# Optimization experiments

Measured on AMD Instinct MI355X. Metric: run time of the kernel, lower is better.

Reference implementation:

```python
import math
import jax, jax.numpy as jnp
import numpy as np

D_MODEL = 1024
N_HEADS = 16
D_K = D_MODEL // N_HEADS


def _alibi_slopes(n_heads):
    # Faithful to the torch _get_slopes: slopes[i] = 2**(-8 + i), subsampled if
    # n_heads is not a power of two.
    power = 2 ** math.ceil(math.log2(n_heads))
    slopes = np.array([2.0 ** (-8 + i) for i in range(power)], dtype=np.float32)
    if n_heads != power:
        ratio = power // n_heads
        slopes = slopes[np.arange(0, power, ratio)][:n_heads]
    return jnp.asarray(slopes)


def setup_inputs() -> dict:
    key = jax.random.key(0)
    ks = jax.random.split(key, 11)
    B, S, D = 2, 2048, D_MODEL
    w = 0.02  # weight init scale
    return {
        "query": jax.random.normal(ks[0], (B, S, D), jnp.float32),
        "key": jax.random.normal(ks[1], (B, S, D), jnp.float32),
        "value": jax.random.normal(ks[2], (B, S, D), jnp.float32),
        "Wq": jax.random.normal(ks[3], (D, D), jnp.float32) * w,
        "bq": jax.random.normal(ks[4], (D,), jnp.float32) * w,
        "Wk": jax.random.normal(ks[5], (D, D), jnp.float32) * w,
        "bk": jax.random.normal(ks[6], (D,), jnp.float32) * w,
        "Wv": jax.random.normal(ks[7], (D, D), jnp.float32) * w,
        "bv": jax.random.normal(ks[8], (D,), jnp.float32) * w,
        "Wo": jax.random.normal(ks[9], (D, D), jnp.float32) * w,
        "bo": jax.random.normal(ks[10], (D,), jnp.float32) * w,
    }


def reference(query, key, value, Wq, bq, Wk, bk, Wv, bv, Wo, bo):
    B, Sq, D = query.shape
    Sk = key.shape[1]
    H, dk = N_HEADS, D_K

    # projections (torch Linear: x @ W.T + b)
    q = (query @ Wq.T + bq).reshape(B, Sq, H, dk).transpose(0, 2, 1, 3)  # [B,H,Sq,dk]
    k = (key @ Wk.T + bk).reshape(B, Sk, H, dk).transpose(0, 2, 1, 3)    # [B,H,Sk,dk]
    v = (value @ Wv.T + bv).reshape(B, Sk, H, dk).transpose(0, 2, 1, 3)  # [B,H,Sk,dk]

    scores = jnp.einsum("bhqd,bhkd->bhqk", q, k) / jnp.sqrt(jnp.float32(dk))

    # ALiBi bias: slopes[h] * (i - j), non-causal path (is_causal=False)
    dist = (jnp.arange(Sq)[:, None] - jnp.arange(Sk)[None, :]).astype(scores.dtype)
    slopes = _alibi_slopes(H)
    scores = scores + slopes[None, :, None, None] * dist[None, None, :, :]

    attn = jax.nn.softmax(scores, axis=-1)
    out = jnp.einsum("bhqk,bhkd->bhqd", attn, v)          # [B,H,Sq,dk]
    out = out.transpose(0, 2, 1, 3).reshape(B, Sq, D)     # [B,Sq,D]
    return out @ Wo.T + bo
```

## Files before the change

kernel.cpp:

```cpp
#include <hip/hip_runtime.h>

typedef __bf16 bf16_t;
typedef bf16_t bf16x8 __attribute__((ext_vector_type(8)));
typedef float f32x4 __attribute__((ext_vector_type(4)));
typedef float f32x16 __attribute__((ext_vector_type(16)));
typedef unsigned short u16x4 __attribute__((ext_vector_type(4)));
typedef unsigned int u32x4v __attribute__((ext_vector_type(4)));
typedef unsigned int u32;

#define DEV static __device__ __forceinline__


DEV unsigned short f2bf(float f) {
  unsigned int u = __builtin_bit_cast(unsigned int, f);
  u = (u + 0x7fffu + ((u >> 16) & 1u)) >> 16;
  return (unsigned short)u;
}

DEV float fexp2(float x) {
  float r;
  asm("v_exp_f32 %0, %1" : "=v"(r) : "v"(x));
  return r;
}

DEV u32 cvtpk(float lo, float hi_) {
  u32 r;
  asm("v_cvt_pk_bf16_f32 %0, %1, %2" : "=v"(r) : "v"(lo), "v"(hi_));
  return r;
}

DEV void plswap(u32& a, u32& b) {
  asm("v_permlane32_swap_b32 %0, %1" : "+v"(a), "+v"(b));
}

DEV void async_ld16(const unsigned short* gsrc, unsigned short* lbase, int lane) {
#if __has_builtin(__builtin_amdgcn_global_load_lds)
  __builtin_amdgcn_global_load_lds(
      (const __attribute__((address_space(1))) unsigned int*)(const void*)gsrc,
      (__attribute__((address_space(3))) unsigned int*)(void*)lbase, 16, 0, 0);
#else
  *reinterpret_cast<u32x4v*>(reinterpret_cast<char*>(lbase) + lane * 16) =
      *reinterpret_cast<const u32x4v*>(gsrc);
#endif
}


DEV void cvt_body(const float* __restrict__ src, unsigned short* __restrict__ dst, int i) {
  const float4* s = reinterpret_cast<const float4*>(src) + (size_t)i * 2;
  float4 a = s[0], c = s[1];
  u16x4 lo = {f2bf(a.x), f2bf(a.y), f2bf(a.z), f2bf(a.w)};
  u16x4 hi = {f2bf(c.x), f2bf(c.y), f2bf(c.z), f2bf(c.w)};
  u16x4* d = reinterpret_cast<u16x4*>(dst) + (size_t)i * 2;
  d[0] = lo;
  d[1] = hi;
}

__global__ __launch_bounds__(256) void cvt_all(
    const float* __restrict__ q, const float* __restrict__ k, const float* __restrict__ v,
    const float* __restrict__ Wq, const float* __restrict__ Wk, const float* __restrict__ Wv,
    const float* __restrict__ Wo, unsigned short* dq, unsigned short* dk, unsigned short* dv,
    unsigned short* dWq, unsigned short* dWk, unsigned short* dWv, unsigned short* dWo,
    unsigned* __restrict__ nb2z) {
  const int bid = blockIdx.x;
  if (nb2z != nullptr && bid == 0 && threadIdx.x < 64) nb2z[threadIdx.x] = 0u;
  const float* src;
  unsigned short* dst;
  int i;
  if (bid < 6144) {
    const int z = bid >> 11;
    src = z == 0 ? q : z == 1 ? k : v;
    dst = z == 0 ? dq : z == 1 ? dk : dv;
    i = (bid & 2047) * 256 + threadIdx.x;
  } else {
    const int z = (bid - 6144) >> 9;
    src = z == 0 ? Wq : z == 1 ? Wk : z == 2 ? Wv : Wo;
    dst = z == 0 ? dWq : z == 1 ? dWk : z == 2 ? dWv : dWo;
    i = ((bid - 6144) & 511) * 256 + threadIdx.x;
  }
  cvt_body(src, dst, i);
}


DEV void mfma_step(const unsigned short* lA, const unsigned short* lB, int lane, int wm, int wn,
                   f32x4 acc[4][4]) {
#pragma unroll
  for (int kk = 0; kk < 2; ++kk) {
    bf16x8 af[4], bfr[4];
#pragma unroll
    for (int f = 0; f < 4; ++f) {
      const int rowA = wm * 64 + f * 16 + (lane & 15);
      const int cA = (kk * 4 + (lane >> 4)) ^ (rowA & 7);
      af[f] = *reinterpret_cast<const bf16x8*>(lA + rowA * 64 + cA * 8);
      const int rowB = wn * 64 + f * 16 + (lane & 15);
      const int cB = (kk * 4 + (lane >> 4)) ^ (rowB & 7);
      bfr[f] = *reinterpret_cast<const bf16x8*>(lB + rowB * 64 + cB * 8);
    }
#pragma unroll
    for (int i = 0; i < 4; ++i)
#pragma unroll
      for (int j = 0; j < 4; ++j)
        acc[i][j] = __builtin_amdgcn_mfma_f32_16x16x32_bf16(af[i], bfr[j], acc[i][j], 0, 0, 0);
  }
}

DEV void gemm_core(const unsigned short* __restrict__ X, const unsigned short* __restrict__ W,
                   unsigned short* lA0, unsigned short* lA1, unsigned short* lB0,
                   unsigned short* lB1, int bm0, int bn0, int lane, int wv, int wm, int wn,
                   f32x4 acc[4][4]) {
  const unsigned short* pa[4];
  const unsigned short* pb[4];
#pragma unroll
  for (int r = 0; r < 4; ++r) {
    const int row = (r * 4 + wv) * 8 + (lane >> 3);
    const int chunk = (lane & 7) ^ (row & 7);
    pa[r] = X + (size_t)(bm0 + row) * 1024 + chunk * 8;
    pb[r] = W + (size_t)(bn0 + row) * 1024 + chunk * 8;
  }
#pragma unroll
  for (int r = 0; r < 4; ++r) {
    async_ld16(pa[r], lA0 + (r * 4 + wv) * 512, lane);
    async_ld16(pb[r], lB0 + (r * 4 + wv) * 512, lane);
  }
  __syncthreads();
#pragma unroll
  for (int kt = 0; kt < 16; ++kt) {
    const unsigned short* lA = (kt & 1) ? lA1 : lA0;
    const unsigned short* lB = (kt & 1) ? lB1 : lB0;
    unsigned short* nA = (kt & 1) ? lA0 : lA1;
    unsigned short* nB = (kt & 1) ? lB0 : lB1;
    if (kt < 15) {
#pragma unroll
      for (int r = 0; r < 4; ++r) {
        async_ld16(pa[r] + (kt + 1) * 64, nA + (r * 4 + wv) * 512, lane);
        async_ld16(pb[r] + (kt + 1) * 64, nB + (r * 4 + wv) * 512, lane);
      }
    }
    mfma_step(lA, lB, lane, wm, wn, acc);
    __syncthreads();
  }
}


__global__ __launch_bounds__(256) void gemm_qkv_kernel(
    const unsigned short* __restrict__ Xq, const unsigned short* __restrict__ Xk,
    const unsigned short* __restrict__ Xv, const unsigned short* __restrict__ Wq,
    const unsigned short* __restrict__ Wk, const unsigned short* __restrict__ Wv,
    const float* __restrict__ bq, const float* __restrict__ bk, const float* __restrict__ bv,
    unsigned short* __restrict__ Qp, unsigned short* __restrict__ Kp,
    unsigned short* __restrict__ Vp, unsigned* __restrict__ nb2) {
  __shared__ unsigned short lA[2][8192];
  __shared__ unsigned short lB[2][8192];
  const unsigned short* X;
  const unsigned short* W;
  const float* bias;
  unsigned short* dst;
  if (blockIdx.z == 0) { X = Xq; W = Wq; bias = bq; dst = Qp; }
  else if (blockIdx.z == 1) { X = Xk; W = Wk; bias = bk; dst = Kp; }
  else { X = Xv; W = Wv; bias = bv; dst = Vp; }
  const bool zV = (blockIdx.z == 2);
  const bool zK = (blockIdx.z == 1) && (nb2 != nullptr);
  const int lane = threadIdx.x & 63, wv = threadIdx.x >> 6;
  const int wm = wv >> 1, wn = wv & 1;
  const int bm0 = blockIdx.x * 128, bn0 = blockIdx.y * 128;
  f32x4 acc[4][4] = {};
  gemm_core(X, W, lA[0], lA[1], lB[0], lB[1], bm0, bn0, lane, wv, wm, wn, acc);
  float rowmax = 0.0f;
#pragma unroll
  for (int i = 0; i < 4; ++i) {
    const int mbase = bm0 + wm * 64 + i * 16 + ((lane >> 4) << 2);
#pragma unroll
    for (int r = 0; r < 4; ++r) {
      const int m = mbase + r;
      const int b = m >> 11, s = m & 2047;
      float ssp = 0.0f;
#pragma unroll
      for (int j = 0; j < 4; ++j) {
        const int n = bn0 + wn * 64 + j * 16 + (lane & 15);
        const float val = acc[i][j][r] + bias[n];
        const unsigned short v16 = f2bf(val);
        const int h = n >> 6, d = n & 63;
        if (zV)
          dst[((size_t)(b * 16 + h) * 64 + d) * 2048 + s] = v16;
        else
          dst[((size_t)(b * 16 + h) * 2048 + s) * 64 + d] = v16;
        ssp = __builtin_fmaf(val, val, ssp);
      }
      if (zK) {
        ssp += __shfl_xor(ssp, 1);
        ssp += __shfl_xor(ssp, 2);
        ssp += __shfl_xor(ssp, 4);
        ssp += __shfl_xor(ssp, 8);
        rowmax = fmaxf(rowmax, ssp);
      }
    }
  }
  if (zK) {
    rowmax = fmaxf(rowmax, __shfl_xor(rowmax, 16));
    rowmax = fmaxf(rowmax, __shfl_xor(rowmax, 32));
    if (lane == 0) {
      const int bh = (bm0 >> 11) * 16 + blockIdx.y * 2 + wn;
      atomicMax(nb2 + bh, __float_as_uint(rowmax));
    }
  }
}


__global__ __launch_bounds__(256) void gemm_out_kernel(const unsigned short* __restrict__ X,
                                                       const unsigned short* __restrict__ W,
                                                       const float* __restrict__ bias,
                                                       float* __restrict__ out) {
  __shared__ unsigned short lA[2][8192];
  __shared__ unsigned short lB[2][8192];
  const int lane = threadIdx.x & 63, wv = threadIdx.x >> 6;
  const int wm = wv >> 1, wn = wv & 1;
  const int bm0 = blockIdx.x * 128, bn0 = blockIdx.y * 128;
  f32x4 acc[4][4] = {};
  gemm_core(X, W, lA[0], lA[1], lB[0], lB[1], bm0, bn0, lane, wv, wm, wn, acc);
#pragma unroll
  for (int i = 0; i < 4; ++i) {
    const int mbase = bm0 + wm * 64 + i * 16 + ((lane >> 4) << 2);
#pragma unroll
    for (int j = 0; j < 4; ++j) {
      const int n = bn0 + wn * 64 + j * 16 + (lane & 15);
      const float bia = bias[n];
#pragma unroll
      for (int r = 0; r < 4; ++r) out[(size_t)(mbase + r) * 1024 + n] = acc[i][j][r] + bia;
    }
  }
}


__global__ __launch_bounds__(256) void knorm_kernel(const unsigned short* __restrict__ Kp,
                                                    unsigned* __restrict__ nb2) {
  const int bh = blockIdx.y;
  const int s = blockIdx.x * 256 + threadIdx.x;
  const u32x4v* row = reinterpret_cast<const u32x4v*>(Kp + ((size_t)bh * 2048 + s) * 64);
  float ss = 0.0f;
#pragma unroll
  for (int c = 0; c < 8; ++c) {
    u32x4v u = row[c];
#pragma unroll
    for (int e = 0; e < 4; ++e) {
      const float lo = __builtin_bit_cast(float, u[e] << 16);
      const float hi = __builtin_bit_cast(float, u[e] & 0xFFFF0000u);
      ss = __builtin_fmaf(lo, lo, ss);
      ss = __builtin_fmaf(hi, hi, ss);
    }
  }
#pragma unroll
  for (int off = 1; off <= 32; off <<= 1) ss = fmaxf(ss, __shfl_xor(ss, off));
  if ((threadIdx.x & 63) == 0) atomicMax(nb2 + bh, __float_as_uint(ss));
}


DEV void stage_tile64(const unsigned short* __restrict__ Gbase, size_t stride, int colbase,
                      unsigned short* lbuf, int lane, int wv) {
#pragma unroll
  for (int i = 0; i < 4; ++i) {
    const int r = i * 16 + wv * 8 + (lane >> 3);
    const int chunk = (lane & 7) ^ (r & 7);
    async_ld16(Gbase + (size_t)r * stride + colbase + chunk * 8, lbuf + (i * 16 + wv * 8) * 64,
               lane);
  }
}

__global__ __launch_bounds__(128) void attn_split_kernel(
    const unsigned short* __restrict__ Qp, const unsigned short* __restrict__ Kp,
    const unsigned short* __restrict__ VTp, const unsigned* __restrict__ nb2,
    float* __restrict__ ML, float* __restrict__ Opart, int Ct, int nsplit) {
  __shared__ unsigned short Kb[2][64 * 64];
  __shared__ unsigned short Vb[2][64 * 64];
  __shared__ float sred[4];
  const int lane = threadIdx.x & 63, wv = threadIdx.x >> 6;
  const int lq = lane & 31, hi = lane >> 5;
  const int qt = blockIdx.x, sp = blockIdx.y, bh = blockIdx.z;
  const int h = bh & 15;
  const int idx = bh * 32 + qt;
  const float L2E = 1.4426950408889634f;
  const float slope2 = ldexpf(L2E, h - 8);
  const float SC2 = 0.125f * L2E;
  const int t0 = sp * Ct;
  float* mlb = ML + ((size_t)idx * nsplit + sp) * 128;
  const size_t headoff = (size_t)bh * 2048 * 64;
  const unsigned short* Qh = Qp + headoff;
  const unsigned short* Kh = Kp + headoff;
  const unsigned short* VTh = VTp + headoff;
  const int q_glob = qt * 64 + wv * 32 + lq;

  float cb0[16], cb1[16];
#pragma unroll
  for (int r = 0; r < 16; ++r) {
    cb0[r] = -slope2 * (float)(4 * hi + (r & 3) + 8 * (r >> 2));
    cb1[r] = cb0[r] - slope2 * 32.0f;
  }

  bf16x8 qf[4];
#pragma unroll
  for (int tt = 0; tt < 4; ++tt)
    qf[tt] = *reinterpret_cast<const bf16x8*>(Qh + (size_t)q_glob * 64 + tt * 16 + hi * 8);

  stage_tile64(Kh + (size_t)(t0 * 64) * 64, 64, 0, Kb[0], lane, wv);
  stage_tile64(VTh, 2048, t0 * 64, Vb[0], lane, wv);

  float qq = 0.0f;
#pragma unroll
  for (int tt = 0; tt < 4; ++tt)
#pragma unroll
    for (int e = 0; e < 8; ++e) {
      const float x = (float)qf[tt][e];
      qq = __builtin_fmaf(x, x, qq);
    }
  qq += __shfl_xor(qq, 32);
#pragma unroll
  for (int off = 1; off <= 16; off <<= 1) qq = fmaxf(qq, __shfl_xor(qq, off));
  {
    f32x16 s0 = {}, s1 = {};
#pragma unroll
    for (int tt = 0; tt < 4; ++tt) {
      bf16x8 k0 = *reinterpret_cast<const bf16x8*>(Kh + (size_t)lq * 64 + tt * 16 + hi * 8);
      s0 = __builtin_amdgcn_mfma_f32_32x32x16_bf16(k0, qf[tt], s0, 0, 0, 0);
      bf16x8 k1 =
          *reinterpret_cast<const bf16x8*>(Kh + (size_t)(32 + lq) * 64 + tt * 16 + hi * 8);
      s1 = __builtin_amdgcn_mfma_f32_32x32x16_bf16(k1, qf[tt], s1, 0, 0, 0);
    }
    float zmax = -3.0e38f;
#pragma unroll
    for (int r = 0; r < 16; ++r) {
      const float x0 = __builtin_fmaf(s0[r], SC2, cb0[r]);
      const float x1 = __builtin_fmaf(s1[r], SC2, cb1[r]);
      zmax = fmaxf(zmax, fmaxf(x0, x1));
    }
    zmax = fmaxf(zmax, __shfl_xor(zmax, 32));
    float zmin = zmax;
#pragma unroll
    for (int off = 1; off <= 16; off <<= 1) zmin = fminf(zmin, __shfl_xor(zmin, off));
    if (lane == 0) {
      sred[wv] = zmin;
      sred[2 + wv] = qq;
    }
  }
  __syncthreads();
  const float m_floor = fminf(sred[0], sred[1]);
  const float qn = sqrtf(fmaxf(sred[2], sred[3]));
  const float blt = qn * sqrtf(__uint_as_float(nb2[bh])) * SC2;
  const float tf = (blt - m_floor + 34.0f) / (slope2 * 64.0f);
  const int T_act = min(32, (int)tf + 1);
  const int nt = min(Ct, T_act - t0);
  if (nt <= 0) {
    mlb[threadIdx.x] = threadIdx.x < 64 ? -3.0e38f : 0.0f;
    return;
  }
  float* ob = Opart + ((size_t)idx * nsplit + sp) * 4096;

  f32x16 acc0 = {}, acc1 = {};
  float m_run = m_floor, l_run = 0.0f;

  for (int ti = 0; ti < nt; ++ti) {
    const int kv0 = (t0 + ti) * 64;
    const float s2k = slope2 * (float)kv0;
    const unsigned short* Kc = Kb[ti & 1];
    const unsigned short* Vc = Vb[ti & 1];
    if (ti + 1 < nt) {
      stage_tile64(Kh + (size_t)(kv0 + 64) * 64, 64, 0, Kb[(ti + 1) & 1], lane, wv);
      stage_tile64(VTh, 2048, kv0 + 64, Vb[(ti + 1) & 1], lane, wv);
    }
    f32x16 s0 = {}, s1 = {};
    __builtin_amdgcn_s_setprio(1);
#pragma unroll
    for (int tt = 0; tt < 4; ++tt) {
      {
        const int row = lq;
        const int ch = (tt * 2 + hi) ^ (row & 7);
        bf16x8 kf = *reinterpret_cast<const bf16x8*>(Kc + row * 64 + ch * 8);
        s0 = __builtin_amdgcn_mfma_f32_32x32x16_bf16(kf, qf[tt], s0, 0, 0, 0);
      }
      {
        const int row = 32 + lq;
        const int ch = (tt * 2 + hi) ^ (row & 7);
        bf16x8 kf = *reinterpret_cast<const bf16x8*>(Kc + row * 64 + ch * 8);
        s1 = __builtin_amdgcn_mfma_f32_32x32x16_bf16(kf, qf[tt], s1, 0, 0, 0);
      }
    }
    __builtin_amdgcn_s_setprio(0);
    float zmax = -3.0e38f;
#pragma unroll
    for (int r = 0; r < 16; ++r) {
      s0[r] = __builtin_fmaf(s0[r], SC2, cb0[r]);
      s1[r] = __builtin_fmaf(s1[r], SC2, cb1[r]);
      zmax = fmaxf(zmax, fmaxf(s0[r], s1[r]));
    }
    zmax = fmaxf(zmax, __shfl_xor(zmax, 32));
    const float tmax_true = zmax - s2k;
    if (__any(tmax_true > m_run + 8.0f)) {
      const float m_new = fmaxf(m_run, tmax_true);
      const float alpha = fexp2(m_run - m_new);
      m_run = m_new;
      l_run *= alpha;
      acc0 *= alpha;
      acc1 *= alpha;
    }
    const float mm = m_run + s2k;
    float ps0 = 0.0f, ps1 = 0.0f;
#pragma unroll
    for (int r = 0; r < 16; ++r) {
      const float p0 = fexp2(s0[r] - mm);
      const float p1 = fexp2(s1[r] - mm);
      s0[r] = p0;
      s1[r] = p1;
      ps0 += p0;
      ps1 += p1;
    }
    float psum = ps0 + ps1;
    psum += __shfl_xor(psum, 32);
    l_run += psum;
    bf16x8 pf[4];
#pragma unroll
    for (int half = 0; half < 2; ++half) {
      u32 w0 = cvtpk(s0[half * 8 + 0], s0[half * 8 + 1]);
      u32 w2 = cvtpk(s0[half * 8 + 4], s0[half * 8 + 5]);
      plswap(w0, w2);
      u32 w1 = cvtpk(s0[half * 8 + 2], s0[half * 8 + 3]);
      u32 w3 = cvtpk(s0[half * 8 + 6], s0[half * 8 + 7]);
      plswap(w1, w3);
      u32x4v ww = {w0, w1, w2, w3};
      pf[half] = __builtin_bit_cast(bf16x8, ww);
    }
#pragma unroll
    for (int half = 0; half < 2; ++half) {
      u32 w0 = cvtpk(s1[half * 8 + 0], s1[half * 8 + 1]);
      u32 w2 = cvtpk(s1[half * 8 + 4], s1[half * 8 + 5]);
      plswap(w0, w2);
      u32 w1 = cvtpk(s1[half * 8 + 2], s1[half * 8 + 3]);
      u32 w3 = cvtpk(s1[half * 8 + 6], s1[half * 8 + 7]);
      plswap(w1, w3);
      u32x4v ww = {w0, w1, w2, w3};
      pf[2 + half] = __builtin_bit_cast(bf16x8, ww);
    }
    __builtin_amdgcn_s_setprio(1);
#pragma unroll
    for (int tt = 0; tt < 4; ++tt) {
      {
        const int row = lq;
        const int ch = (tt * 2 + hi) ^ (row & 7);
        bf16x8 vf = *reinterpret_cast<const bf16x8*>(Vc + row * 64 + ch * 8);
        acc0 = __builtin_amdgcn_mfma_f32_32x32x16_bf16(vf, pf[tt], acc0, 0, 0, 0);
      }
      {
        const int row = 32 + lq;
        const int ch = (tt * 2 + hi) ^ (row & 7);
        bf16x8 vf = *reinterpret_cast<const bf16x8*>(Vc + row * 64 + ch * 8);
        acc1 = __builtin_amdgcn_mfma_f32_32x32x16_bf16(vf, pf[tt], acc1, 0, 0, 0);
      }
    }
    __builtin_amdgcn_s_setprio(0);
    __syncthreads();
  }
  const int qloc = wv * 32 + lq;
  if (hi == 0) {
    mlb[qloc] = m_run;
    mlb[64 + qloc] = l_run;
  }
#pragma unroll
  for (int g = 0; g < 4; ++g) {
    f32x4 w0, w1;
#pragma unroll
    for (int e = 0; e < 4; ++e) {
      w0[e] = acc0[g * 4 + e];
      w1[e] = acc1[g * 4 + e];
    }
    *reinterpret_cast<f32x4*>(ob + qloc * 64 + g * 8 + 4 * hi) = w0;
    *reinterpret_cast<f32x4*>(ob + qloc * 64 + 32 + g * 8 + 4 * hi) = w1;
  }
}


__global__ __launch_bounds__(256) void attn_combine(const float* __restrict__ ML,
                                                    const float* __restrict__ Opart,
                                                    unsigned short* __restrict__ Ob, int nsplit) {
  const int idx = blockIdx.x;
  const int bh = idx >> 5, qt = idx & 31;
  const int h = bh & 15, b = bh >> 4;
  const int q = threadIdx.x >> 2, d0 = (threadIdx.x & 3) * 16;
  const float* mlb = ML + (size_t)idx * nsplit * 128;
  const float* ob = Opart + (size_t)idx * nsplit * 4096;
  float m_g = -3.0e38f;
  for (int s = 0; s < nsplit; ++s) m_g = fmaxf(m_g, mlb[s * 128 + q]);
  float l = 0.0f;
  f32x4 acc[4] = {};
  for (int s = 0; s < nsplit; ++s) {
    const float ms = mlb[s * 128 + q], ls = mlb[s * 128 + 64 + q];
    const float w = fexp2(ms - m_g);
    const float wl = w * ls;
    if (wl > 0.0f) {
      l += wl;
      const f32x4* src = reinterpret_cast<const f32x4*>(ob + (size_t)s * 4096 + q * 64 + d0);
#pragma unroll
      for (int j = 0; j < 4; ++j) {
        f32x4 v = src[j];
#pragma unroll
        for (int e = 0; e < 4; ++e) acc[j][e] = __builtin_fmaf(w, v[e], acc[j][e]);
      }
    }
  }
  const float invl = 1.0f / l;
  unsigned short* orow = Ob + ((size_t)(b * 2048 + qt * 64 + q)) * 1024 + h * 64 + d0;
#pragma unroll
  for (int j = 0; j < 4; ++j) {
    u16x4 pk;
#pragma unroll
    for (int e = 0; e < 4; ++e) pk[e] = f2bf(acc[j][e] * invl);
    *reinterpret_cast<u16x4*>(orow + j * 4) = pk;
  }
}


extern "C" void kernel_launch(void* const* d_in, const int* in_sizes, int n_in, void* d_out,
                              int out_size, void* d_ws, size_t ws_size, hipStream_t stream) {
  const float* q = (const float*)d_in[0];
  const float* k = (const float*)d_in[1];
  const float* v = (const float*)d_in[2];
  const float* Wq = (const float*)d_in[3];
  const float* bq = (const float*)d_in[4];
  const float* Wk = (const float*)d_in[5];
  const float* bk = (const float*)d_in[6];
  const float* Wv = (const float*)d_in[7];
  const float* bv = (const float*)d_in[8];
  const float* Wo = (const float*)d_in[9];
  const float* bo = (const float*)d_in[10];

  char* ws = (char*)d_ws;
  const size_t MB = 1024 * 1024;
  unsigned short* qb = (unsigned short*)(ws + 0 * MB);
  unsigned short* kb = (unsigned short*)(ws + 8 * MB);
  unsigned short* vb = (unsigned short*)(ws + 16 * MB);
  unsigned short* Wqb = (unsigned short*)(ws + 24 * MB);
  unsigned short* Wkb = (unsigned short*)(ws + 26 * MB);
  unsigned short* Wvb = (unsigned short*)(ws + 28 * MB);
  unsigned short* Wob = (unsigned short*)(ws + 30 * MB);
  unsigned short* Qp = (unsigned short*)(ws + 32 * MB);
  unsigned short* Kp = (unsigned short*)(ws + 40 * MB);
  unsigned short* VTp = (unsigned short*)(ws + 48 * MB);
  unsigned short* Obf = (unsigned short*)(ws + 0 * MB);

  int nsplit;
  float *ML, *Opart;
  unsigned* nb2;
  bool fold_knorm;
  if (ws_size >= (size_t)121 * MB) nsplit = 4;
  else if (ws_size >= (size_t)89 * MB) nsplit = 2;
  else nsplit = 1;
  if (ws_size >= (size_t)73 * MB) {
    fold_knorm = true;
    nb2 = (unsigned*)(ws + 56 * MB);
    ML = (float*)(ws + 26 * MB + 65536);
    Opart = (float*)(ws + 56 * MB + 4096);
  } else {
    fold_knorm = false;
    nsplit = 1;
    nb2 = (unsigned*)(ws + 26 * MB);
    ML = (float*)(ws + 26 * MB + 65536);
    Opart = (float*)(ws + 8 * MB);
  }
  const int Ct = 32 / nsplit;

  cvt_all<<<8192, 256, 0, stream>>>(q, k, v, Wq, Wk, Wv, Wo, qb, kb, vb, Wqb, Wkb, Wvb, Wob,
                                    fold_knorm ? nb2 : nullptr);
  gemm_qkv_kernel<<<dim3(32, 8, 3), 256, 0, stream>>>(qb, kb, vb, Wqb, Wkb, Wvb, bq, bk, bv, Qp,
                                                      Kp, VTp, fold_knorm ? nb2 : nullptr);
  if (!fold_knorm) {
    hipMemsetAsync(nb2, 0, 64 * sizeof(unsigned), stream);
    knorm_kernel<<<dim3(8, 32), 256, 0, stream>>>(Kp, nb2);
  }
  attn_split_kernel<<<dim3(32, nsplit, 32), 128, 0, stream>>>(Qp, Kp, VTp, nb2, ML, Opart, Ct,
                                                              nsplit);
  attn_combine<<<1024, 256, 0, stream>>>(ML, Opart, Obf, nsplit);
  gemm_out_kernel<<<dim3(32, 8), 256, 0, stream>>>(Obf, Wob, bo, (float*)d_out);
}
```

Measured before the change: 124.4 us.

## Enlarge QKV projection GEMM tiles to 256x256 with 512-thread blocks

The QKV projection GEMM moves from 128x128 tiles with 4 waves to 256x256 tiles with 8 waves, each wave computing a 128x64 sub-tile. This halves global loads per output element and raises arithmetic intensity per LDS stage. In exchange, LDS use doubles to 128KB per block and the grid shrinks to 192 blocks, fewer than the CU count, so occupancy and load balance may suffer. The output GEMM keeps the old 128-tile path, its loop no longer fully unrolled.

New measurement: 135.9 us. 9.3% more time.

```diff
diff --git a/kernel.cpp b/kernel.cpp
--- a/kernel.cpp
+++ b/kernel.cpp
@@ -81,75 +81,74 @@
 }
 
 
-DEV void mfma_step(const unsigned short* lA, const unsigned short* lB, int lane, int wm, int wn,
-                   f32x4 acc[4][4]) {
+DEV void stage_tile256(const unsigned short* __restrict__ G, int row0, int k0,
+                       unsigned short* lbuf, int lane, int w) {
+#pragma unroll
+  for (int r = 0; r < 4; ++r) {
+    const int row = r * 64 + w * 8 + (lane >> 3);
+    const int chunk = (lane & 7) ^ (row & 7);
+    async_ld16(G + (size_t)(row0 + row) * 1024 + k0 + chunk * 8, lbuf + (r * 64 + w * 8) * 64,
+               lane);
+  }
+}
+
+DEV void mfma_step256(const unsigned short* lA, const unsigned short* lB, int lane, int wm,
+                      int wn, f32x4 acc[8][4]) {
 #pragma unroll
   for (int kk = 0; kk < 2; ++kk) {
-    bf16x8 af[4], bfr[4];
-#pragma unroll
-    for (int f = 0; f < 4; ++f) {
-      const int rowA = wm * 64 + f * 16 + (lane & 15);
+    bf16x8 af[8], bfr[4];
+#pragma unroll
+    for (int f = 0; f < 8; ++f) {
+      const int rowA = wm * 128 + f * 16 + (lane & 15);
       const int cA = (kk * 4 + (lane >> 4)) ^ (rowA & 7);
       af[f] = *reinterpret_cast<const bf16x8*>(lA + rowA * 64 + cA * 8);
-      const int rowB = wn * 64 + f * 16 + (lane & 15);
+    }
+#pragma unroll
+    for (int j = 0; j < 4; ++j) {
+      const int rowB = wn * 64 + j * 16 + (lane & 15);
       const int cB = (kk * 4 + (lane >> 4)) ^ (rowB & 7);
-      bfr[f] = *reinterpret_cast<const bf16x8*>(lB + rowB * 64 + cB * 8);
-    }
-#pragma unroll
-    for (int i = 0; i < 4; ++i)
+      bfr[j] = *reinterpret_cast<const bf16x8*>(lB + rowB * 64 + cB * 8);
+    }
+#pragma unroll
+    for (int i = 0; i < 8; ++i)
 #pragma unroll
       for (int j = 0; j < 4; ++j)
         acc[i][j] = __builtin_amdgcn_mfma_f32_16x16x32_bf16(af[i], bfr[j], acc[i][j], 0, 0, 0);
   }
 }
 
-DEV void gemm_core(const unsigned short* __restrict__ X, const unsigned short* __restrict__ W,
-                   unsigned short* lA0, unsigned short* lA1, unsigned short* lB0,
-                   unsigned short* lB1, int bm0, int bn0, int lane, int wv, int wm, int wn,
-                   f32x4 acc[4][4]) {
-  const unsigned short* pa[4];
-  const unsigned short* pb[4];
-#pragma unroll
-  for (int r = 0; r < 4; ++r) {
-    const int row = (r * 4 + wv) * 8 + (lane >> 3);
-    const int chunk = (lane & 7) ^ (row & 7);
-    pa[r] = X + (size_t)(bm0 + row) * 1024 + chunk * 8;
-    pb[r] = W + (size_t)(bn0 + row) * 1024 + chunk * 8;
-  }
-#pragma unroll
-  for (int r = 0; r < 4; ++r) {
-    async_ld16(pa[r], lA0 + (r * 4 + wv) * 512, lane);
-    async_ld16(pb[r], lB0 + (r * 4 + wv) * 512, lane);
-  }
+DEV void gemm_core256(const unsigned short* __restrict__ X, const unsigned short* __restrict__ W,
+                      unsigned short* lA0, unsigned short* lA1, unsigned short* lB0,
+                      unsigned short* lB1, int bm0, int bn0, int lane, int w, int wm, int wn,
+                      f32x4 acc[8][4]) {
+  stage_tile256(X, bm0, 0, lA0, lane, w);
+  stage_tile256(W, bn0, 0, lB0, lane, w);
   __syncthreads();
-#pragma unroll
+#pragma unroll 2
   for (int kt = 0; kt < 16; ++kt) {
     const unsigned short* lA = (kt & 1) ? lA1 : lA0;
     const unsigned short* lB = (kt & 1) ? lB1 : lB0;
     unsigned short* nA = (kt & 1) ? lA0 : lA1;
     unsigned short* nB = (kt & 1) ? lB0 : lB1;
     if (kt < 15) {
-#pragma unroll
-      for (int r = 0; r < 4; ++r) {
-        async_ld16(pa[r] + (kt + 1) * 64, nA + (r * 4 + wv) * 512, lane);
-        async_ld16(pb[r] + (kt + 1) * 64, nB + (r * 4 + wv) * 512, lane);
-      }
-    }
-    mfma_step(lA, lB, lane, wm, wn, acc);
+      stage_tile256(X, bm0, (kt + 1) * 64, nA, lane, w);
+      stage_tile256(W, bn0, (kt + 1) * 64, nB, lane, w);
+    }
+    mfma_step256(lA, lB, lane, wm, wn, acc);
     __syncthreads();
   }
 }
 
 
-__global__ __launch_bounds__(256) void gemm_qkv_kernel(
+__global__ __launch_bounds__(512, 2) void gemm_qkv_kernel(
     const unsigned short* __restrict__ Xq, const unsigned short* __restrict__ Xk,
     const unsigned short* __restrict__ Xv, const unsigned short* __restrict__ Wq,
     const unsigned short* __restrict__ Wk, const unsigned short* __restrict__ Wv,
     const float* __restrict__ bq, const float* __restrict__ bk, const float* __restrict__ bv,
     unsigned short* __restrict__ Qp, unsigned short* __restrict__ Kp,
     unsigned short* __restrict__ Vp, unsigned* __restrict__ nb2) {
-  __shared__ unsigned short lA[2][8192];
-  __shared__ unsigned short lB[2][8192];
+  __shared__ unsigned short lA[2][16384];
+  __shared__ unsigned short lB[2][16384];
   const unsigned short* X;
   const unsigned short* W;
   const float* bias;
@@ -159,15 +158,15 @@
   else { X = Xv; W = Wv; bias = bv; dst = Vp; }
   const bool zV = (blockIdx.z == 2);
   const bool zK = (blockIdx.z == 1) && (nb2 != nullptr);
-  const int lane = threadIdx.x & 63, wv = threadIdx.x >> 6;
-  const int wm = wv >> 1, wn = wv & 1;
-  const int bm0 = blockIdx.x * 128, bn0 = blockIdx.y * 128;
-  f32x4 acc[4][4] = {};
-  gemm_core(X, W, lA[0], lA[1], lB[0], lB[1], bm0, bn0, lane, wv, wm, wn, acc);
+  const int lane = threadIdx.x & 63, w = threadIdx.x >> 6;
+  const int wm = w >> 2, wn = w & 3;
+  const int bm0 = blockIdx.x * 256, bn0 = blockIdx.y * 256;
+  f32x4 acc[8][4] = {};
+  gemm_core256(X, W, lA[0], lA[1], lB[0], lB[1], bm0, bn0, lane, w, wm, wn, acc);
   float rowmax = 0.0f;
 #pragma unroll
-  for (int i = 0; i < 4; ++i) {
-    const int mbase = bm0 + wm * 64 + i * 16 + ((lane >> 4) << 2);
+  for (int i = 0; i < 8; ++i) {
+    const int mbase = bm0 + wm * 128 + i * 16 + ((lane >> 4) << 2);
 #pragma unroll
     for (int r = 0; r < 4; ++r) {
       const int m = mbase + r;
@@ -198,9 +197,64 @@
     rowmax = fmaxf(rowmax, __shfl_xor(rowmax, 16));
     rowmax = fmaxf(rowmax, __shfl_xor(rowmax, 32));
     if (lane == 0) {
-      const int bh = (bm0 >> 11) * 16 + blockIdx.y * 2 + wn;
+      const int bh = (bm0 >> 11) * 16 + blockIdx.y * 4 + wn;
       atomicMax(nb2 + bh, __float_as_uint(rowmax));
     }
+  }
+}
+
+
+DEV void stage_b128(const unsigned short* __restrict__ G, int row0, int k0,
+                    unsigned short* lbuf, int lane, int wv) {
+#pragma unroll
+  for (int r = 0; r < 4; ++r) {
+    const int rowB = (r * 4 + wv) * 8 + (lane >> 3);
+    const int chunk = (lane & 7) ^ (rowB & 7);
+    async_ld16(G + (size_t)(row0 + rowB) * 1024 + k0 + chunk * 8, lbuf + (r * 4 + wv) * 512,
+               lane);
+  }
+}
+
+DEV void mfma_step(const unsigned short* lA, const unsigned short* lB, int lane, int wm, int wn,
+                   f32x4 acc[4][4]) {
+#pragma unroll
+  for (int kk = 0; kk < 2; ++kk) {
+    bf16x8 af[4], bfr[4];
+#pragma unroll
+    for (int f = 0; f < 4; ++f) {
+      const int rowA = wm * 64 + f * 16 + (lane & 15);
+      const int cA = (kk * 4 + (lane >> 4)) ^ (rowA & 7);
+      af[f] = *reinterpret_cast<const bf16x8*>(lA + rowA * 64 + cA * 8);
+      const int rowB = wn * 64 + f * 16 + (lane & 15);
+      const int cB = (kk * 4 + (lane >> 4)) ^ (rowB & 7);
+      bfr[f] = *reinterpret_cast<const bf16x8*>(lB + rowB * 64 + cB * 8);
+    }
+#pragma unroll
+    for (int i = 0; i < 4; ++i)
+#pragma unroll
+      for (int j = 0; j < 4; ++j)
+        acc[i][j] = __builtin_amdgcn_mfma_f32_16x16x32_bf16(af[i], bfr[j], acc[i][j], 0, 0, 0);
+  }
+}
+
+DEV void gemm_core(const unsigned short* __restrict__ X, const unsigned short* __restrict__ W,
+                   unsigned short* lA0, unsigned short* lA1, unsigned short* lB0,
+                   unsigned short* lB1, int bm0, int bn0, int lane, int wv, int wm, int wn,
+                   f32x4 acc[4][4]) {
+  stage_b128(X, bm0, 0, lA0, lane, wv);
+  stage_b128(W, bn0, 0, lB0, lane, wv);
+  __syncthreads();
+  for (int kt = 0; kt < 16; ++kt) {
+    const unsigned short* lA = (kt & 1) ? lA1 : lA0;
+    const unsigned short* lB = (kt & 1) ? lB1 : lB0;
+    unsigned short* nA = (kt & 1) ? lA0 : lA1;
+    unsigned short* nB = (kt & 1) ? lB0 : lB1;
+    if (kt < 15) {
+      stage_b128(X, bm0, (kt + 1) * 64, nA, lane, wv);
+      stage_b128(W, bn0, (kt + 1) * 64, nB, lane, wv);
+    }
+    mfma_step(lA, lB, lane, wm, wn, acc);
+    __syncthreads();
   }
 }
 
@@ -565,7 +619,7 @@
 
   cvt_all<<<8192, 256, 0, stream>>>(q, k, v, Wq, Wk, Wv, Wo, qb, kb, vb, Wqb, Wkb, Wvb, Wob,
                                     fold_knorm ? nb2 : nullptr);
-  gemm_qkv_kernel<<<dim3(32, 8, 3), 256, 0, stream>>>(qb, kb, vb, Wqb, Wkb, Wvb, bq, bk, bv, Qp,
+  gemm_qkv_kernel<<<dim3(16, 4, 3), 512, 0, stream>>>(qb, kb, vb, Wqb, Wkb, Wvb, bq, bk, bv, Qp,
                                                       Kp, VTp, fold_knorm ? nb2 : nullptr);
   if (!fold_knorm) {
     hipMemsetAsync(nb2, 0, 64 * sizeof(unsigned), stream);
```

## Rewrite QKV projection GEMM as 256x256 tile, 8-wave ping-pong pipeline

Applied to the files above, without the earlier changes.

The QKV projection GEMM moves from 128x128 tiles with 4 waves and a double buffer to 256x256 tiles with 8 waves. Half-tiles are staged through a four-slot LDS ring, and loads are interleaved with MFMA groups between barriers. Explicit vmcnt waits, s_setprio around the MFMA bursts and sched_barrier fences keep memory traffic overlapped with compute. The larger tile gives more reuse per LDS load, but the grid shrinks to 192 blocks at one block per CU, which may leave some of the 256 CUs idle. It also uses more LDS and registers.

After: 145.2 us. 1.17x slower.

```diff
diff --git a/kernel.cpp b/kernel.cpp
--- a/kernel.cpp
+++ b/kernel.cpp
@@ -81,75 +81,56 @@
 }
 
 
-DEV void mfma_step(const unsigned short* lA, const unsigned short* lB, int lane, int wm, int wn,
-                   f32x4 acc[4][4]) {
-#pragma unroll
-  for (int kk = 0; kk < 2; ++kk) {
-    bf16x8 af[4], bfr[4];
-#pragma unroll
-    for (int f = 0; f < 4; ++f) {
-      const int rowA = wm * 64 + f * 16 + (lane & 15);
-      const int cA = (kk * 4 + (lane >> 4)) ^ (rowA & 7);
-      af[f] = *reinterpret_cast<const bf16x8*>(lA + rowA * 64 + cA * 8);
-      const int rowB = wn * 64 + f * 16 + (lane & 15);
-      const int cB = (kk * 4 + (lane >> 4)) ^ (rowB & 7);
-      bfr[f] = *reinterpret_cast<const bf16x8*>(lB + rowB * 64 + cB * 8);
-    }
-#pragma unroll
-    for (int i = 0; i < 4; ++i)
-#pragma unroll
-      for (int j = 0; j < 4; ++j)
-        acc[i][j] = __builtin_amdgcn_mfma_f32_16x16x32_bf16(af[i], bfr[j], acc[i][j], 0, 0, 0);
-  }
-}
-
-DEV void gemm_core(const unsigned short* __restrict__ X, const unsigned short* __restrict__ W,
-                   unsigned short* lA0, unsigned short* lA1, unsigned short* lB0,
-                   unsigned short* lB1, int bm0, int bn0, int lane, int wv, int wm, int wn,
-                   f32x4 acc[4][4]) {
-  const unsigned short* pa[4];
-  const unsigned short* pb[4];
-#pragma unroll
-  for (int r = 0; r < 4; ++r) {
-    const int row = (r * 4 + wv) * 8 + (lane >> 3);
+DEV void stage_half(const unsigned short* __restrict__ G, int grow0, int k0,
+                    unsigned short* hbuf, int tid) {
+  const int lane = tid & 63, w = tid >> 6;
+#pragma unroll
+  for (int l = 0; l < 2; ++l) {
+    const int row = l * 64 + w * 8 + (lane >> 3);
     const int chunk = (lane & 7) ^ (row & 7);
-    pa[r] = X + (size_t)(bm0 + row) * 1024 + chunk * 8;
-    pb[r] = W + (size_t)(bn0 + row) * 1024 + chunk * 8;
-  }
-#pragma unroll
-  for (int r = 0; r < 4; ++r) {
-    async_ld16(pa[r], lA0 + (r * 4 + wv) * 512, lane);
-    async_ld16(pb[r], lB0 + (r * 4 + wv) * 512, lane);
-  }
-  __syncthreads();
-#pragma unroll
-  for (int kt = 0; kt < 16; ++kt) {
-    const unsigned short* lA = (kt & 1) ? lA1 : lA0;
-    const unsigned short* lB = (kt & 1) ? lB1 : lB0;
-    unsigned short* nA = (kt & 1) ? lA0 : lA1;
-    unsigned short* nB = (kt & 1) ? lB0 : lB1;
-    if (kt < 15) {
-#pragma unroll
-      for (int r = 0; r < 4; ++r) {
-        async_ld16(pa[r] + (kt + 1) * 64, nA + (r * 4 + wv) * 512, lane);
-        async_ld16(pb[r] + (kt + 1) * 64, nB + (r * 4 + wv) * 512, lane);
-      }
-    }
-    mfma_step(lA, lB, lane, wm, wn, acc);
-    __syncthreads();
-  }
-}
-
-
-__global__ __launch_bounds__(256) void gemm_qkv_kernel(
+    async_ld16(G + (size_t)(grow0 + row) * 1024 + k0 + chunk * 8,
+               hbuf + (l * 64 + w * 8) * 64, lane);
+  }
+}
+
+DEV void read_a2(const unsigned short* hb, int pi, int lane, bf16x8 af[2][2]) {
+#pragma unroll
+  for (int ii = 0; ii < 2; ++ii)
+#pragma unroll
+    for (int kk = 0; kk < 2; ++kk) {
+      const int lrow = pi * 32 + ii * 16 + (lane & 15);
+      const int ch = (kk * 4 + (lane >> 4)) ^ (lrow & 7);
+      af[ii][kk] = *reinterpret_cast<const bf16x8*>(hb + lrow * 64 + ch * 8);
+    }
+}
+
+DEV void mfma16(const bf16x8 af[2][2], const bf16x8 bf[4][2], f32x4 (*accp)[4]) {
+  __builtin_amdgcn_s_setprio(1);
+#pragma unroll
+  for (int ii = 0; ii < 2; ++ii)
+#pragma unroll
+    for (int j = 0; j < 4; ++j)
+#pragma unroll
+      for (int kk = 0; kk < 2; ++kk)
+        accp[ii][j] =
+            __builtin_amdgcn_mfma_f32_16x16x32_bf16(af[ii][kk], bf[j][kk], accp[ii][j], 0, 0, 0);
+  __builtin_amdgcn_s_setprio(0);
+}
+
+DEV void barrier_fence() {
+  __builtin_amdgcn_s_barrier();
+  __builtin_amdgcn_sched_barrier(0);
+}
+
+__global__ __launch_bounds__(512, 1) void gemm_qkv_kernel(
     const unsigned short* __restrict__ Xq, const unsigned short* __restrict__ Xk,
     const unsigned short* __restrict__ Xv, const unsigned short* __restrict__ Wq,
     const unsigned short* __restrict__ Wk, const unsigned short* __restrict__ Wv,
     const float* __restrict__ bq, const float* __restrict__ bk, const float* __restrict__ bv,
     unsigned short* __restrict__ Qp, unsigned short* __restrict__ Kp,
     unsigned short* __restrict__ Vp, unsigned* __restrict__ nb2) {
-  __shared__ unsigned short lA[2][8192];
-  __shared__ unsigned short lB[2][8192];
+  __shared__ unsigned short Ar[4][8192];
+  __shared__ unsigned short Br[4][8192];
   const unsigned short* X;
   const unsigned short* W;
   const float* bias;
@@ -159,15 +140,70 @@
   else { X = Xv; W = Wv; bias = bv; dst = Vp; }
   const bool zV = (blockIdx.z == 2);
   const bool zK = (blockIdx.z == 1) && (nb2 != nullptr);
-  const int lane = threadIdx.x & 63, wv = threadIdx.x >> 6;
-  const int wm = wv >> 1, wn = wv & 1;
-  const int bm0 = blockIdx.x * 128, bn0 = blockIdx.y * 128;
-  f32x4 acc[4][4] = {};
-  gemm_core(X, W, lA[0], lA[1], lB[0], lB[1], bm0, bn0, lane, wv, wm, wn, acc);
+  const int tid = threadIdx.x;
+  const int lane = tid & 63, w = tid >> 6;
+  const int wm = w >> 2, wn = w & 3;
+  const int bm0 = blockIdx.x * 256, bn0 = blockIdx.y * 256;
+  f32x4 acc[8][4] = {};
+
+  stage_half(W, bn0, 0, &Br[0][0], tid);
+  stage_half(W, bn0 + 128, 0, &Br[1][0], tid);
+  stage_half(X, bm0, 0, &Ar[0][0], tid);
+  stage_half(X, bm0 + 128, 0, &Ar[1][0], tid);
+  stage_half(W, bn0, 64, &Br[2][0], tid);
+  stage_half(W, bn0 + 128, 64, &Br[3][0], tid);
+  asm volatile("s_waitcnt vmcnt(4)" ::: "memory");
+  barrier_fence();
+
+  for (int t = 0; t < 16; ++t) {
+    const int s0 = (2 * t) & 3, s1 = (2 * t + 1) & 3;
+    const unsigned short* hbA = wm ? &Ar[s1][0] : &Ar[s0][0];
+    const unsigned short* hbB = (wn < 2) ? &Br[s0][0] : &Br[s1][0];
+    unsigned short* nA0 = &Ar[(s0 + 2) & 3][0];
+    unsigned short* nA1 = &Ar[(s1 + 2) & 3][0];
+    unsigned short* nB0 = &Br[s0][0];
+    unsigned short* nB1 = &Br[s1][0];
+    if (t + 1 < 16) stage_half(X, bm0, (t + 1) * 64, nA0, tid);
+    bf16x8 bf[4][2];
+    {
+      const int lr0 = (wn & 1) * 64;
+#pragma unroll
+      for (int j = 0; j < 4; ++j)
+#pragma unroll
+        for (int kk = 0; kk < 2; ++kk) {
+          const int lrow = lr0 + j * 16 + (lane & 15);
+          const int ch = (kk * 4 + (lane >> 4)) ^ (lrow & 7);
+          bf[j][kk] = *reinterpret_cast<const bf16x8*>(hbB + lrow * 64 + ch * 8);
+        }
+    }
+    bf16x8 af[2][2];
+    read_a2(hbA, 0, lane, af);
+    mfma16(af, bf, &acc[0]);
+    barrier_fence();
+    if (t + 1 < 16) stage_half(X, bm0 + 128, (t + 1) * 64, nA1, tid);
+    if (t + 2 < 16) stage_half(W, bn0, (t + 2) * 64, nB0, tid);
+    read_a2(hbA, 1, lane, af);
+    mfma16(af, bf, &acc[2]);
+    barrier_fence();
+    if (t + 2 < 16) stage_half(W, bn0 + 128, (t + 2) * 64, nB1, tid);
+    read_a2(hbA, 2, lane, af);
+    mfma16(af, bf, &acc[4]);
+    barrier_fence();
+    read_a2(hbA, 3, lane, af);
+    mfma16(af, bf, &acc[6]);
+    if (t < 15) {
+      if (t == 14)
+        asm volatile("s_waitcnt vmcnt(0)" ::: "memory");
+      else
+        asm volatile("s_waitcnt vmcnt(4)" ::: "memory");
+      barrier_fence();
+    }
+  }
+
   float rowmax = 0.0f;
 #pragma unroll
-  for (int i = 0; i < 4; ++i) {
-    const int mbase = bm0 + wm * 64 + i * 16 + ((lane >> 4) << 2);
+  for (int i = 0; i < 8; ++i) {
+    const int mbase = bm0 + wm * 128 + i * 16 + ((lane >> 4) << 2);
 #pragma unroll
     for (int r = 0; r < 4; ++r) {
       const int m = mbase + r;
@@ -198,12 +234,71 @@
     rowmax = fmaxf(rowmax, __shfl_xor(rowmax, 16));
     rowmax = fmaxf(rowmax, __shfl_xor(rowmax, 32));
     if (lane == 0) {
-      const int bh = (bm0 >> 11) * 16 + blockIdx.y * 2 + wn;
+      const int bh = (bm0 >> 11) * 16 + blockIdx.y * 4 + wn;
       atomicMax(nb2 + bh, __float_as_uint(rowmax));
     }
   }
 }
 
+
+DEV void mfma_step(const unsigned short* lA, const unsigned short* lB, int lane, int wm, int wn,
+                   f32x4 acc[4][4]) {
+#pragma unroll
+  for (int kk = 0; kk < 2; ++kk) {
+    bf16x8 af[4], bfr[4];
+#pragma unroll
+    for (int f = 0; f < 4; ++f) {
+      const int rowA = wm * 64 + f * 16 + (lane & 15);
+      const int cA = (kk * 4 + (lane >> 4)) ^ (rowA & 7);
+      af[f] = *reinterpret_cast<const bf16x8*>(lA + rowA * 64 + cA * 8);
+      const int rowB = wn * 64 + f * 16 + (lane & 15);
+      const int cB = (kk * 4 + (lane >> 4)) ^ (rowB & 7);
+      bfr[f] = *reinterpret_cast<const bf16x8*>(lB + rowB * 64 + cB * 8);
+    }
+#pragma unroll
+    for (int i = 0; i < 4; ++i)
+#pragma unroll
+      for (int j = 0; j < 4; ++j)
+        acc[i][j] = __builtin_amdgcn_mfma_f32_16x16x32_bf16(af[i], bfr[j], acc[i][j], 0, 0, 0);
+  }
+}
+
+DEV void gemm_core(const unsigned short* __restrict__ X, const unsigned short* __restrict__ W,
+                   unsigned short* lA0, unsigned short* lA1, unsigned short* lB0,
+                   unsigned short* lB1, int bm0, int bn0, int lane, int wv, int wm, int wn,
+                   f32x4 acc[4][4]) {
+  const unsigned short* pa[4];
+  const unsigned short* pb[4];
+#pragma unroll
+  for (int r = 0; r < 4; ++r) {
+    const int row = (r * 4 + wv) * 8 + (lane >> 3);
+    const int chunk = (lane & 7) ^ (row & 7);
+    pa[r] = X + (size_t)(bm0 + row) * 1024 + chunk * 8;
+    pb[r] = W + (size_t)(bn0 + row) * 1024 + chunk * 8;
+  }
+#pragma unroll
+  for (int r = 0; r < 4; ++r) {
+    async_ld16(pa[r], lA0 + (r * 4 + wv) * 512, lane);
+    async_ld16(pb[r], lB0 + (r * 4 + wv) * 512, lane);
+  }
+  __syncthreads();
+#pragma unroll
+  for (int kt = 0; kt < 16; ++kt) {
+    const unsigned short* lA = (kt & 1) ? lA1 : lA0;
+    const unsigned short* lB = (kt & 1) ? lB1 : lB0;
+    unsigned short* nA = (kt & 1) ? lA0 : lA1;
+    unsigned short* nB = (kt & 1) ? lB0 : lB1;
+    if (kt < 15) {
+#pragma unroll
+      for (int r = 0; r < 4; ++r) {
+        async_ld16(pa[r] + (kt + 1) * 64, nA + (r * 4 + wv) * 512, lane);
+        async_ld16(pb[r] + (kt + 1) * 64, nB + (r * 4 + wv) * 512, lane);
+      }
+    }
+    mfma_step(lA, lB, lane, wm, wn, acc);
+    __syncthreads();
+  }
+}
 
 __global__ __launch_bounds__(256) void gemm_out_kernel(const unsigned short* __restrict__ X,
                                                        const unsigned short* __restrict__ W,
@@ -565,7 +660,7 @@
 
   cvt_all<<<8192, 256, 0, stream>>>(q, k, v, Wq, Wk, Wv, Wo, qb, kb, vb, Wqb, Wkb, Wvb, Wob,
                                     fold_knorm ? nb2 : nullptr);
-  gemm_qkv_kernel<<<dim3(32, 8, 3), 256, 0, stream>>>(qb, kb, vb, Wqb, Wkb, Wvb, bq, bk, bv, Qp,
+  gemm_qkv_kernel<<<dim3(16, 4, 3), 512, 0, stream>>>(qb, kb, vb, Wqb, Wkb, Wvb, bq, bk, bv, Qp,
                                                       Kp, VTp, fold_knorm ? nb2 : nullptr);
   if (!fold_knorm) {
     hipMemsetAsync(nb2, 0, 64 * sizeof(unsigned), stream);
```
